# Kernel tuning notes

Measured on AMD Instinct MI355X. Metric: run time of the kernel, lower is better.

## Reference

```python
import jax, jax.numpy as jnp
import numpy as np

N = 4096
LAT, COND, PH, E = 64, 219, 20, 8
H, OUT = 512, 171
GIN = PH * 2 + LAT  # 104


def setup_inputs() -> dict:
    key = jax.random.key(0)
    ks = jax.random.split(key, 15)
    s = 0.05  # small init scale for stability under ELU/softmax
    return {
        "latent": jax.random.normal(ks[0], (N, LAT), jnp.float32),
        "condition": jax.random.normal(ks[1], (N, COND), jnp.float32),
        "phase": jax.random.normal(ks[2], (N, PH, 2), jnp.float32),
        "gate_w1": jax.random.normal(ks[3], (GIN, 128), jnp.float32) * s,
        "gate_b1": jnp.zeros((128,), jnp.float32),
        "gate_w2": jax.random.normal(ks[4], (128, 128), jnp.float32) * s,
        "gate_b2": jnp.zeros((128,), jnp.float32),
        "gate_w3": jax.random.normal(ks[5], (128, E), jnp.float32) * s,
        "gate_b3": jnp.zeros((E,), jnp.float32),
        "w0": jax.random.normal(ks[6], (E, COND + LAT, H), jnp.float32) * s,
        "b0": jnp.zeros((E, H), jnp.float32),
        "w1": jax.random.normal(ks[7], (E, H + LAT, H), jnp.float32) * s,
        "b1": jnp.zeros((E, H), jnp.float32),
        "w2": jax.random.normal(ks[8], (E, H, OUT), jnp.float32) * s,
        "b2": jnp.zeros((E, OUT), jnp.float32),
    }


def _moe_linear(x, coeff, W, b):
    # Per-sample expert blend: out_n = sum_e coeff[n,e] * (x_n @ W[e] + b[e])
    # (mathematically identical to blending weights first, but avoids
    #  materializing an [N, in, out] per-sample weight tensor)
    h = jnp.einsum('ni,eio->neo', x, W) + b[None]  # [N, E, out]
    return jnp.einsum('ne,neo->no', coeff, h)


def reference(latent, condition, phase,
              gate_w1, gate_b1, gate_w2, gate_b2, gate_w3, gate_b3,
              w0, b0, w1, b1, w2, b2):
    elu = jax.nn.elu
    # gate network: softmax over experts
    g = jnp.concatenate([phase.reshape(phase.shape[0], -1), latent], axis=-1)
    g = elu(g @ gate_w1 + gate_b1)
    g = elu(g @ gate_w2 + gate_b2)
    coeff = jax.nn.softmax(g @ gate_w3 + gate_b3, axis=-1)  # [N, E]
    # expert-blended MLP with latent re-concatenation
    x = jnp.concatenate([condition, latent], axis=-1)
    x = elu(_moe_linear(x, coeff, w0, b0))
    x = jnp.concatenate([x, latent], axis=-1)
    x = elu(_moe_linear(x, coeff, w1, b1))
    pred_pose = _moe_linear(x, coeff, w2, b2)
    return pred_pose, coeff
```

## Files before the change

kernel.cpp:

```cpp
#include <hip/hip_runtime.h>
#include <hip/hip_bf16.h>

#define NR 4096

typedef float f32x4 __attribute__((ext_vector_type(4)));
typedef __bf16 bf16x8 __attribute__((ext_vector_type(8)));

typedef __attribute__((address_space(1))) unsigned int u32_g;
typedef __attribute__((address_space(3))) unsigned int u32_l;

__device__ __forceinline__ void gl_lds16(const void* g, void* l) {
  __builtin_amdgcn_global_load_lds((const u32_g*)g, (u32_l*)l, 16, 0, 0);
}


__device__ void wstage32(const float* __restrict__ w, __hip_bfloat16* __restrict__ out,
                         int Kin, int KT, int Oin, int u, char* LDS)
{
  int ob = u / (KT * 2);
  int rem = u - ob * (KT * 2);
  int T = rem >> 1, s = rem & 1;
  float* t = (float*)LDS;
  const int tid = threadIdx.x;
  const int kbase = T * 64 + s * 32;

  if (Oin == 512) {
#pragma unroll
    for (int i = 0; i < 8; ++i) {
      int idx = i * 256 + tid;
      int row = idx >> 3, c4 = idx & 7;
      int e = row >> 5, kk = row & 31;
      int k = kbase + kk;
      float4 v = {0.f, 0.f, 0.f, 0.f};
      if (k < Kin) v = *(const float4*)&w[((size_t)e * Kin + k) * 512 + ob * 32 + c4 * 4];
      t[row * 33 + c4 * 4 + 0] = v.x;
      t[row * 33 + c4 * 4 + 1] = v.y;
      t[row * 33 + c4 * 4 + 2] = v.z;
      t[row * 33 + c4 * 4 + 3] = v.w;
    }
  } else {
#pragma unroll
    for (int i = 0; i < 8; ++i) {
      int idx = i * 256 + tid;
      int row = idx >> 3, c4 = idx & 7;
      int e = row >> 5, kk = row & 31;
      int k = kbase + kk;
#pragma unroll
      for (int j = 0; j < 4; ++j) {
        int o = ob * 32 + c4 * 4 + j;
        float f = (k < Kin && o < Oin) ? w[((size_t)e * Kin + k) * (size_t)Oin + o] : 0.f;
        t[row * 33 + c4 * 4 + j] = f;
      }
    }
  }
  __syncthreads();
  {
    int p = tid;
    int e = ((p >> 4) & 3) * 2 + (p & 1);
    int oo = ((p >> 6) & 3) * 8 + ((p >> 1) & 7);
    size_t segbase = (((size_t)ob * KT + T) * 2 + s) * 16384;
#pragma unroll
    for (int g = 0; g < 4; ++g) {
      bf16x8 v;
#pragma unroll
      for (int e8 = 0; e8 < 8; ++e8) v[e8] = (__bf16)t[(e * 32 + g * 8 + e8) * 33 + oo];
      *(bf16x8*)((char*)out + segbase + g * 4096 + (size_t)p * 16) = v;
    }
  }
  __syncthreads();
}

__device__ void x0unit(int u, const float* __restrict__ cond, const float* __restrict__ lat,
                       __hip_bfloat16* __restrict__ out)
{
  int c = u * 256 + threadIdx.x;
  int RB = c / 10240;
  int r1 = c - RB * 10240;
  int T = r1 >> 11, r2 = r1 & 2047;
  int n = RB * 256 + (r2 & 255);
  int k0 = T * 64 + (r2 >> 10) * 32 + ((r2 >> 8) & 3) * 8;
  bf16x8 v;
#pragma unroll
  for (int e = 0; e < 8; ++e) {
    int k = k0 + e;
    float f = (k < 219) ? cond[(size_t)n * 219 + k]
            : (k < 283) ? lat[(size_t)n * 64 + (k - 219)] : 0.f;
    v[e] = (__bf16)f;
  }
  *(bf16x8*)((char*)out + (size_t)c * 16) = v;
}

__device__ void x1lat(int u, const float* __restrict__ lat, __hip_bfloat16* __restrict__ out)
{
  int c = u * 256 + threadIdx.x;
  int RB = c >> 11, r2 = c & 2047;
  int n = RB * 256 + (r2 & 255);
  int k0 = (r2 >> 10) * 32 + ((r2 >> 8) & 3) * 8;
  bf16x8 v;
#pragma unroll
  for (int e = 0; e < 8; ++e) v[e] = (__bf16)lat[(size_t)n * 64 + k0 + e];
  size_t off = ((size_t)RB * 9 + 8) * 32768 + (size_t)r2 * 16;
  *(bf16x8*)((char*)out + off) = v;
}

__device__ void gate16(int gb, const float* __restrict__ phs, const float* __restrict__ lat,
                       const float* __restrict__ gw1, const float* __restrict__ gb1,
                       const float* __restrict__ gw2, const float* __restrict__ gb2,
                       const float* __restrict__ gw3, const float* __restrict__ gb3,
                       float* __restrict__ coeff, char* LDS)
{
  float* aT  = (float*)LDS;
  float* h1T = (float*)(LDS + 10240);
  float* w3L = (float*)(LDS + 20480);
  const int tid = threadIdx.x;
  const int n0 = gb * 16;

  for (int i = tid; i < 104 * 16; i += 256) {
    int k = i >> 4, r = i & 15;
    aT[k * 20 + r] = (k < 40) ? phs[(size_t)(n0 + r) * 40 + k]
                              : lat[(size_t)(n0 + r) * 64 + (k - 40)];
  }
  ((float4*)w3L)[tid] = ((const float4*)gw3)[tid];
  __syncthreads();

  const int col = tid & 127, rh = tid >> 7;
  {
    float acc[8] = {};
#pragma unroll 8
    for (int k = 0; k < 104; ++k) {
      float w = gw1[k * 128 + col];
#pragma unroll
      for (int r = 0; r < 8; ++r) acc[r] += aT[k * 20 + rh * 8 + r] * w;
    }
    float bb = gb1[col];
#pragma unroll
    for (int r = 0; r < 8; ++r) {
      float v = acc[r] + bb;
      h1T[col * 20 + rh * 8 + r] = v > 0.f ? v : expm1f(v);
    }
  }
  __syncthreads();
  {
    float acc[8] = {};
#pragma unroll 8
    for (int k = 0; k < 128; ++k) {
      float w = gw2[k * 128 + col];
#pragma unroll
      for (int r = 0; r < 8; ++r) acc[r] += h1T[k * 20 + rh * 8 + r] * w;
    }
    float bb = gb2[col];
#pragma unroll
    for (int r = 0; r < 8; ++r) {
      float v = acc[r] + bb;
      aT[col * 20 + rh * 8 + r] = v > 0.f ? v : expm1f(v);
    }
  }
  __syncthreads();
  if (tid < 128) {
    int row = tid >> 3, e = tid & 7;
    float a3 = 0.f;
#pragma unroll 8
    for (int k = 0; k < 128; ++k) a3 += aT[k * 20 + row] * w3L[k * 8 + e];
    float lgt = a3 + gb3[e];
    float m = lgt;
    m = fmaxf(m, __shfl_xor(m, 1));
    m = fmaxf(m, __shfl_xor(m, 2));
    m = fmaxf(m, __shfl_xor(m, 4));
    float ex = expf(lgt - m);
    float s = ex;
    s += __shfl_xor(s, 1);
    s += __shfl_xor(s, 2);
    s += __shfl_xor(s, 4);
    coeff[(size_t)(n0 + row) * 8 + e] = ex / s;
  }
}

__global__ __launch_bounds__(256) void prepG(
    const float* __restrict__ latent, const float* __restrict__ condition,
    const float* __restrict__ phase,
    const float* __restrict__ gw1, const float* __restrict__ gb1,
    const float* __restrict__ gw2, const float* __restrict__ gb2,
    const float* __restrict__ gw3, const float* __restrict__ gb3,
    const float* __restrict__ w0, const float* __restrict__ w1, const float* __restrict__ w2,
    __hip_bfloat16* x0s, __hip_bfloat16* x1s,
    __hip_bfloat16* w0s, __hip_bfloat16* w1s, __hip_bfloat16* w2s,
    float* coeff)
{
  __shared__ __align__(16) char LDS[33792];
  int b = blockIdx.x;
  if (b < 256) {
    gate16(b, phase, latent, gw1, gb1, gw2, gb2, gw3, gb3, coeff, LDS);
    return;
  }
  b -= 256;
  if (b < 288)       wstage32(w1, w1s, 576, 9, 512, b, LDS);
  else if (b < 448)  wstage32(w0, w0s, 283, 5, 512, b - 288, LDS);
  else if (b < 544)  wstage32(w2, w2s, 512, 8, 171, b - 448, LDS);
  else if (b < 1184) x0unit(b - 544, condition, latent, x0s);
  else {
    int u0 = (b - 1184) * 2;
    x1lat(u0, latent, x1s);
    x1lat(u0 + 1, latent, x1s);
  }
}

template <int KT, int KTD, int MODE, int BYPG>
__global__ __launch_bounds__(512, 4) void gemm_k(
    const __hip_bfloat16* __restrict__ Ap, const __hip_bfloat16* __restrict__ Bp,
    const float* __restrict__ coeff, const float* __restrict__ bias,
    __hip_bfloat16* __restrict__ dstS, float* __restrict__ dstF)
{
  __shared__ __align__(16) char lds[49152];
  const int bid = blockIdx.x;
  const int xcd = bid & 7, r = bid >> 3;
  const int bx = ((xcd & 3) << 3) + (r & 7);
  const int by = (xcd >> 2) * BYPG + (r >> 3);
  const int tid = threadIdx.x;
  const int lane = tid & 63;
  const int wid = tid >> 6;
  const int wr = wid >> 2, wc = wid & 3;
  const int l15 = lane & 15, lg = lane >> 4;
  const int aHalf = (bx & 1) * 2048;

  const char* aG = (const char*)Ap + (size_t)(bx >> 1) * KT * 32768;
  const char* bG = (const char*)Bp + (size_t)by * KT * 32768;

#define STAGE(T)                                                             \
  {                                                                          \
    const char* gA_ = aG + (size_t)(T) * 32768;                              \
    const char* gB_ = bG + (size_t)(T) * 32768;                              \
    _Pragma("unroll") for (int i = 0; i < 2; ++i) {                          \
      int c = i * 512 + tid;                                                 \
      gl_lds16(gA_ + (c >> 9) * 16384 + ((c >> 7) & 3) * 4096 + aHalf        \
                   + (c & 127) * 16,                                         \
               lds + c * 16);                                                \
    }                                                                        \
    _Pragma("unroll") for (int i = 0; i < 4; ++i) {                          \
      int c = i * 512 + tid;                                                 \
      gl_lds16(gB_ + c * 16, lds + 16384 + c * 16);                          \
    }                                                                        \
  }

  f32x4 acc[4][4] = {};

  STAGE(0);
  asm volatile("s_waitcnt vmcnt(0)" ::: "memory");
  __builtin_amdgcn_s_barrier();

#pragma unroll 1
  for (int t = 0; t < KT; ++t) {
#pragma unroll
    for (int s = 0; s < 2; ++s) {
      bf16x8 a[4], b[4];
#pragma unroll
      for (int fm = 0; fm < 4; ++fm)
        a[fm] = *(const bf16x8*)(lds + s * 8192 + lg * 2048
                                 + ((wr << 6) + fm * 16 + l15) * 16);
#pragma unroll
      for (int nf = 0; nf < 4; ++nf)
        b[nf] = *(const bf16x8*)(lds + 16384 + s * 16384 + lg * 4096
                                 + (wc << 10) + nf * 256 + l15 * 16);
#pragma unroll
      for (int fm = 0; fm < 4; ++fm)
#pragma unroll
        for (int nf = 0; nf < 4; ++nf)
          acc[fm][nf] = __builtin_amdgcn_mfma_f32_16x16x32_bf16(a[fm], b[nf], acc[fm][nf], 0, 0, 0);
    }
    if (t + 1 < KT) {
      __builtin_amdgcn_s_barrier();
      STAGE(t + 1);
      asm volatile("s_waitcnt vmcnt(0)" ::: "memory");
      __builtin_amdgcn_s_barrier();
    }
  }
#undef STAGE
  __syncthreads();

  float* cl2 = (float*)lds;
  float* tb  = (float*)(lds + 4352);
  {
#pragma unroll
    for (int i = 0; i < 2; ++i) {
      int idx = i * 512 + tid;
      int e = idx & 7, n = idx >> 3;
      cl2[e * 132 + n] = coeff[((size_t)bx * 128 + n) * 8 + e];
    }
  }
  __syncthreads();
  const int e0 = lane & 1;
  const int o_loc = (wc << 3) + (l15 >> 1);

  if (MODE == 0) {
    float bb[4];
#pragma unroll
    for (int fn = 0; fn < 4; ++fn) bb[fn] = bias[(fn * 2 + e0) * 512 + by * 32 + o_loc];
#pragma unroll
    for (int fm = 0; fm < 4; ++fm) {
#pragma unroll
      for (int r2 = 0; r2 < 4; ++r2) {
        int n_loc = (wr << 6) + fm * 16 + (lg << 2) + r2;
        float s = 0.f;
#pragma unroll
        for (int fn = 0; fn < 4; ++fn)
          s += cl2[(fn * 2 + e0) * 132 + n_loc] * (acc[fm][fn][r2] + bb[fn]);
        s += __shfl_xor(s, 1);
        s = s > 0.f ? s : expm1f(s);
        if ((lane & 1) == (fm & 1)) tb[n_loc * 33 + o_loc] = s;
      }
    }
    __syncthreads();
    {
      int n_loc = tid & 127, c = tid >> 7;
      const float* p = &tb[n_loc * 33 + c * 8];
      bf16x8 v;
#pragma unroll
      for (int j = 0; j < 8; ++j) v[j] = (__bf16)p[j];
      size_t off = (((size_t)(bx >> 1) * KTD + (by >> 1)) * 2 + (by & 1)) * 16384
                 + (size_t)c * 4096 + (size_t)((bx & 1) * 128 + n_loc) * 16;
      *(bf16x8*)((char*)dstS + off) = v;
    }
  } else {
    const int o_g = by * 32 + o_loc;
    if (o_g < 171) {
      float bb[4];
#pragma unroll
      for (int fn = 0; fn < 4; ++fn) bb[fn] = bias[(fn * 2 + e0) * 171 + o_g];
#pragma unroll
      for (int fm = 0; fm < 4; ++fm) {
#pragma unroll
        for (int r2 = 0; r2 < 4; ++r2) {
          int n_loc = (wr << 6) + fm * 16 + (lg << 2) + r2;
          float s = 0.f;
#pragma unroll
          for (int fn = 0; fn < 4; ++fn)
            s += cl2[(fn * 2 + e0) * 132 + n_loc] * (acc[fm][fn][r2] + bb[fn]);
          s += __shfl_xor(s, 1);
          if ((lane & 1) == (fm & 1))
            dstF[(size_t)(bx * 128 + n_loc) * 171 + o_g] = s;
        }
      }
    }
  }
}

extern "C" void kernel_launch(void* const* d_in, const int* in_sizes, int n_in,
                              void* d_out, int out_size, void* d_ws, size_t ws_size,
                              hipStream_t stream)
{
  const float* latent    = (const float*)d_in[0];
  const float* condition = (const float*)d_in[1];
  const float* phase     = (const float*)d_in[2];
  const float* gw1 = (const float*)d_in[3];
  const float* gb1 = (const float*)d_in[4];
  const float* gw2 = (const float*)d_in[5];
  const float* gb2 = (const float*)d_in[6];
  const float* gw3 = (const float*)d_in[7];
  const float* gb3 = (const float*)d_in[8];
  const float* w0  = (const float*)d_in[9];
  const float* b0  = (const float*)d_in[10];
  const float* w1  = (const float*)d_in[11];
  const float* b1  = (const float*)d_in[12];
  const float* w2  = (const float*)d_in[13];
  const float* b2  = (const float*)d_in[14];

  float* out   = (float*)d_out;
  float* coeff = out + (size_t)NR * 171;

  char* ws = (char*)d_ws;
  __hip_bfloat16* x0s = (__hip_bfloat16*)ws; ws += (size_t)16 * 5 * 32768;
  __hip_bfloat16* x1s = (__hip_bfloat16*)ws; ws += (size_t)16 * 9 * 32768;
  __hip_bfloat16* x2s = (__hip_bfloat16*)ws; ws += (size_t)16 * 8 * 32768;
  __hip_bfloat16* w0s = (__hip_bfloat16*)ws; ws += (size_t)16 * 5 * 32768;
  __hip_bfloat16* w1s = (__hip_bfloat16*)ws; ws += (size_t)16 * 9 * 32768;
  __hip_bfloat16* w2s = (__hip_bfloat16*)ws; ws += (size_t)6 * 8 * 32768;

  prepG<<<1504, 256, 0, stream>>>(latent, condition, phase,
                                  gw1, gb1, gw2, gb2, gw3, gb3,
                                  w0, w1, w2,
                                  x0s, x1s, w0s, w1s, w2s, coeff);

  gemm_k<5, 9, 0, 8><<<512, 512, 0, stream>>>(x0s, w0s, coeff, b0, x1s, nullptr);
  gemm_k<9, 8, 0, 8><<<512, 512, 0, stream>>>(x1s, w1s, coeff, b1, x2s, nullptr);
  gemm_k<8, 0, 1, 3><<<192, 512, 0, stream>>>(x2s, w2s, coeff, b2, nullptr, out);
}
```

Before: 74.97 us.

## Split gate network into its own finer-grained kernel separate from staging

Moves the gating MLP out of the combined prep kernel into a dedicated kernel with 128-thread blocks, each handling 4 rows instead of 16, giving 1024 blocks instead of 256 so more CUs work on the serial gate chain. The staging/conversion work becomes its own kernel, and the trailing barrier in the weight staging routine is removed. This adds an extra kernel launch on the same stream, so the gate work no longer overlaps with staging, and each gate block re-reads the gate weights for fewer rows.

```diff
diff --git a/kernel.cpp b/kernel.cpp
--- a/kernel.cpp
+++ b/kernel.cpp
@@ -67,7 +67,6 @@
       *(bf16x8*)((char*)out + segbase + g * 4096 + (size_t)p * 16) = v;
     }
   }
-  __syncthreads();
 }
 
 __device__ void x0unit(int u, const float* __restrict__ cond, const float* __restrict__ lat,
@@ -103,64 +102,84 @@
   *(bf16x8*)((char*)out + off) = v;
 }
 
-__device__ void gate16(int gb, const float* __restrict__ phs, const float* __restrict__ lat,
-                       const float* __restrict__ gw1, const float* __restrict__ gb1,
-                       const float* __restrict__ gw2, const float* __restrict__ gb2,
-                       const float* __restrict__ gw3, const float* __restrict__ gb3,
-                       float* __restrict__ coeff, char* LDS)
-{
-  float* aT  = (float*)LDS;
-  float* h1T = (float*)(LDS + 10240);
-  float* w3L = (float*)(LDS + 20480);
+__global__ __launch_bounds__(256) void stageK(
+    const float* __restrict__ latent, const float* __restrict__ condition,
+    const float* __restrict__ w0, const float* __restrict__ w1, const float* __restrict__ w2,
+    __hip_bfloat16* x0s, __hip_bfloat16* x1s,
+    __hip_bfloat16* w0s, __hip_bfloat16* w1s, __hip_bfloat16* w2s)
+{
+  __shared__ __align__(16) char LDS[33792];
+  int b = blockIdx.x;
+  if (b < 288)       wstage32(w1, w1s, 576, 9, 512, b, LDS);
+  else if (b < 448)  wstage32(w0, w0s, 283, 5, 512, b - 288, LDS);
+  else if (b < 544)  wstage32(w2, w2s, 512, 8, 171, b - 448, LDS);
+  else if (b < 1184) x0unit(b - 544, condition, latent, x0s);
+  else {
+    int u0 = (b - 1184) * 2;
+    x1lat(u0, latent, x1s);
+    x1lat(u0 + 1, latent, x1s);
+  }
+}
+
+__global__ __launch_bounds__(128) void gateK(
+    const float* __restrict__ phs, const float* __restrict__ lat,
+    const float* __restrict__ gw1, const float* __restrict__ gb1,
+    const float* __restrict__ gw2, const float* __restrict__ gb2,
+    const float* __restrict__ gw3, const float* __restrict__ gb3,
+    float* __restrict__ coeff)
+{
+  __shared__ __align__(16) float aT[128 * 8];
+  __shared__ __align__(16) float h1T[128 * 8];
+  __shared__ __align__(16) float w3L[128 * 8];
   const int tid = threadIdx.x;
-  const int n0 = gb * 16;
-
-  for (int i = tid; i < 104 * 16; i += 256) {
-    int k = i >> 4, r = i & 15;
-    aT[k * 20 + r] = (k < 40) ? phs[(size_t)(n0 + r) * 40 + k]
-                              : lat[(size_t)(n0 + r) * 64 + (k - 40)];
-  }
-  ((float4*)w3L)[tid] = ((const float4*)gw3)[tid];
-  __syncthreads();
-
-  const int col = tid & 127, rh = tid >> 7;
+  const int n0 = blockIdx.x * 4;
+
+  for (int i = tid; i < 104 * 4; i += 128) {
+    int k = i >> 2, r = i & 3;
+    aT[k * 8 + r] = (k < 40) ? phs[(size_t)(n0 + r) * 40 + k]
+                             : lat[(size_t)(n0 + r) * 64 + (k - 40)];
+  }
+#pragma unroll
+  for (int i = 0; i < 2; ++i) ((float4*)w3L)[i * 128 + tid] = ((const float4*)gw3)[i * 128 + tid];
+  __syncthreads();
+
   {
-    float acc[8] = {};
+    float acc[4] = {};
 #pragma unroll 8
     for (int k = 0; k < 104; ++k) {
-      float w = gw1[k * 128 + col];
-#pragma unroll
-      for (int r = 0; r < 8; ++r) acc[r] += aT[k * 20 + rh * 8 + r] * w;
-    }
-    float bb = gb1[col];
-#pragma unroll
-    for (int r = 0; r < 8; ++r) {
+      float w = gw1[k * 128 + tid];
+#pragma unroll
+      for (int r = 0; r < 4; ++r) acc[r] += aT[k * 8 + r] * w;
+    }
+    float bb = gb1[tid];
+#pragma unroll
+    for (int r = 0; r < 4; ++r) {
       float v = acc[r] + bb;
-      h1T[col * 20 + rh * 8 + r] = v > 0.f ? v : expm1f(v);
+      h1T[tid * 8 + r] = v > 0.f ? v : expm1f(v);
     }
   }
   __syncthreads();
   {
-    float acc[8] = {};
+    float acc[4] = {};
 #pragma unroll 8
     for (int k = 0; k < 128; ++k) {
-      float w = gw2[k * 128 + col];
-#pragma unroll
-      for (int r = 0; r < 8; ++r) acc[r] += h1T[k * 20 + rh * 8 + r] * w;
-    }
-    float bb = gb2[col];
-#pragma unroll
-    for (int r = 0; r < 8; ++r) {
+      float w = gw2[k * 128 + tid];
+#pragma unroll
+      for (int r = 0; r < 4; ++r) acc[r] += h1T[k * 8 + r] * w;
+    }
+    float bb = gb2[tid];
+#pragma unroll
+    for (int r = 0; r < 4; ++r) {
       float v = acc[r] + bb;
-      aT[col * 20 + rh * 8 + r] = v > 0.f ? v : expm1f(v);
-    }
-  }
-  __syncthreads();
-  if (tid < 128) {
+      aT[tid * 8 + r] = v > 0.f ? v : expm1f(v);
+    }
+  }
+  __syncthreads();
+  if (tid < 32) {
     int row = tid >> 3, e = tid & 7;
     float a3 = 0.f;
 #pragma unroll 8
-    for (int k = 0; k < 128; ++k) a3 += aT[k * 20 + row] * w3L[k * 8 + e];
+    for (int k = 0; k < 128; ++k) a3 += aT[k * 8 + row] * w3L[k * 8 + e];
     float lgt = a3 + gb3[e];
     float m = lgt;
     m = fmaxf(m, __shfl_xor(m, 1));
@@ -172,35 +191,6 @@
     s += __shfl_xor(s, 2);
     s += __shfl_xor(s, 4);
     coeff[(size_t)(n0 + row) * 8 + e] = ex / s;
-  }
-}
-
-__global__ __launch_bounds__(256) void prepG(
-    const float* __restrict__ latent, const float* __restrict__ condition,
-    const float* __restrict__ phase,
-    const float* __restrict__ gw1, const float* __restrict__ gb1,
-    const float* __restrict__ gw2, const float* __restrict__ gb2,
-    const float* __restrict__ gw3, const float* __restrict__ gb3,
-    const float* __restrict__ w0, const float* __restrict__ w1, const float* __restrict__ w2,
-    __hip_bfloat16* x0s, __hip_bfloat16* x1s,
-    __hip_bfloat16* w0s, __hip_bfloat16* w1s, __hip_bfloat16* w2s,
-    float* coeff)
-{
-  __shared__ __align__(16) char LDS[33792];
-  int b = blockIdx.x;
-  if (b < 256) {
-    gate16(b, phase, latent, gw1, gb1, gw2, gb2, gw3, gb3, coeff, LDS);
-    return;
-  }
-  b -= 256;
-  if (b < 288)       wstage32(w1, w1s, 576, 9, 512, b, LDS);
-  else if (b < 448)  wstage32(w0, w0s, 283, 5, 512, b - 288, LDS);
-  else if (b < 544)  wstage32(w2, w2s, 512, 8, 171, b - 448, LDS);
-  else if (b < 1184) x0unit(b - 544, condition, latent, x0s);
-  else {
-    int u0 = (b - 1184) * 2;
-    x1lat(u0, latent, x1s);
-    x1lat(u0 + 1, latent, x1s);
   }
 }
 
@@ -374,10 +364,10 @@
   __hip_bfloat16* w1s = (__hip_bfloat16*)ws; ws += (size_t)16 * 9 * 32768;
   __hip_bfloat16* w2s = (__hip_bfloat16*)ws; ws += (size_t)6 * 8 * 32768;
 
-  prepG<<<1504, 256, 0, stream>>>(latent, condition, phase,
-                                  gw1, gb1, gw2, gb2, gw3, gb3,
-                                  w0, w1, w2,
-                                  x0s, x1s, w0s, w1s, w2s, coeff);
+  stageK<<<1248, 256, 0, stream>>>(latent, condition, w0, w1, w2,
+                                   x0s, x1s, w0s, w1s, w2s);
+
+  gateK<<<1024, 128, 0, stream>>>(phase, latent, gw1, gb1, gw2, gb2, gw3, gb3, coeff);
 
   gemm_k<5, 9, 0, 8><<<512, 512, 0, stream>>>(x0s, w0s, coeff, b0, x1s, nullptr);
   gemm_k<9, 8, 0, 8><<<512, 512, 0, stream>>>(x1s, w1s, coeff, b1, x2s, nullptr);
```

Result: slower. 83.07 us (+10.8%).
